# Optimization experiments

Measured on AMD Instinct MI355X. Metric: run time of the kernel, lower is better.

## Reference

```python
import jax, jax.numpy as jnp
import numpy as np

NUM_DISPARITIES = 64


def setup_inputs() -> dict:
    key = jax.random.key(0)
    k1, k2 = jax.random.split(key)
    B, C, H, W = 4, 32, 256, 512
    left = jax.random.normal(k1, (B, C, H, W), dtype=jnp.float32)
    right = jax.random.normal(k2, (B, C, H, W), dtype=jnp.float32)
    return {"left": left, "right": right}


def cost_volume(left, right, num_disparities):
    # left, right: [B, C, H, W] -> output [B, D, H, W]
    W = left.shape[3]
    wcoord = jnp.arange(W)  # [W]

    def one_disparity(i):
        # right shifted so rs[..., w] == right[..., w - i] for w >= i
        rs = jnp.roll(right, i, axis=3)
        corr = jnp.mean(left * rs, axis=1)  # [B, H, W] channel-mean dot product
        # zero out invalid columns w < i (matches zeros-init + slice write in torch)
        return jnp.where(wcoord >= i, corr, jnp.zeros_like(corr))

    # sequential map over disparities keeps peak memory at one [B,C,H,W] product
    out = jax.lax.map(one_disparity, jnp.arange(num_disparities))  # [D, B, H, W]
    return jnp.transpose(out, (1, 0, 2, 3))  # [B, D, H, W]


def reference(left, right):
    return cost_volume(left, right, NUM_DISPARITIES)
```

## Files before the change

kernel.cpp:

```cpp
#include <hip/hip_runtime.h>


constexpr int Bn = 4, Cn = 32, Hn = 256, Wn = 512, Dn = 64;
constexpr int WT = 4, DT = 16;
constexpr int PAD = 64;
constexpr int STRIDE = PAD + Wn;
constexpr int HW = Hn * Wn;

__global__ __launch_bounds__(512, 4)
void cost_volume_kernel(const float* __restrict__ left,
                        const float* __restrict__ right,
                        float* __restrict__ out)
{
    __shared__ __align__(16) float Rs[Cn * STRIDE];

    const int tid = threadIdx.x;
    const int bh  = blockIdx.x;
    const int b   = bh >> 8;
    const int h   = bh & (Hn - 1);

    const float* Lrow = left  + (b * Cn * Hn + h) * Wn;
    const float* Rrow = right + (b * Cn * Hn + h) * Wn;

    {
        const int c  = tid >> 4;
        const int wq = (tid & 15) << 2;
        *reinterpret_cast<float4*>(&Rs[c * STRIDE + wq]) =
            make_float4(0.f, 0.f, 0.f, 0.f);
    }

    #pragma unroll
    for (int k = 0; k < 8; ++k) {
        const int f = tid + (k << 9);
        const int c = f >> 7;
        const int w = (f & 127) << 2;
        const float4 v = *reinterpret_cast<const float4*>(&Rrow[c * HW + w]);
        *reinterpret_cast<float4*>(&Rs[c * STRIDE + PAD + w]) = v;
    }
    __syncthreads();

    const int tw = tid & 127;
    const int td = tid >> 7;
    const int w0 = tw << 2;
    const int d0 = td << 4;
    const int rbase = PAD + w0 - d0 - 16;

    float acc[DT][WT];
    #pragma unroll
    for (int j = 0; j < DT; ++j)
        #pragma unroll
        for (int i = 0; i < WT; ++i)
            acc[j][i] = 0.f;

    for (int c = 0; c < Cn; ++c) {
        const float4 Lv = *reinterpret_cast<const float4*>(&Lrow[c * HW + w0]);
        const float lv[4] = {Lv.x, Lv.y, Lv.z, Lv.w};

        const float* rp = &Rs[c * STRIDE + rbase];
        float r[20];
        #pragma unroll
        for (int q = 0; q < 5; ++q)
            *reinterpret_cast<float4*>(&r[q * 4]) =
                *reinterpret_cast<const float4*>(&rp[q * 4]);

        #pragma unroll
        for (int j = 0; j < DT; ++j)
            #pragma unroll
            for (int i = 0; i < WT; ++i)
                acc[j][i] = fmaf(lv[i], r[16 + i - j], acc[j][i]);
    }

    constexpr float inv = 1.0f / 32.0f;
    float* op = out + ((b * Dn + d0) * Hn + h) * Wn + w0;
    #pragma unroll
    for (int j = 0; j < DT; ++j) {
        const float4 v = make_float4(acc[j][0] * inv, acc[j][1] * inv,
                                     acc[j][2] * inv, acc[j][3] * inv);
        *reinterpret_cast<float4*>(&op[j * HW]) = v;
    }
}

extern "C" void kernel_launch(void* const* d_in, const int* in_sizes, int n_in,
                              void* d_out, int out_size, void* d_ws, size_t ws_size,
                              hipStream_t stream) {
    const float* left  = (const float*)d_in[0];
    const float* right = (const float*)d_in[1];
    float* out = (float*)d_out;
    cost_volume_kernel<<<dim3(Bn * Hn), dim3(512), 0, stream>>>(left, right, out);
}
```

Before: 249.8 us.

## Pipeline per-wave right-row staging via direct global-to-LDS ring buffers

Replaces the block-wide load of the whole right row into shared memory, and the barrier that follows, with a private three-slot ring buffer for each wave. The ring is filled asynchronously with global_load_lds and synchronised with manual waitcnt instructions, so channel loads overlap the FMA loop and the left-row loads are prefetched two channels ahead. Each wave now covers a 256-wide half-row for 16 disparities. This cuts LDS use from about 74KB to about 37KB, which may allow more blocks per CU. In exchange, each wave redundantly loads the overlapping halo, and correctness depends on the hand-written vmcnt and lgkmcnt counts.

```diff
diff --git a/kernel.cpp b/kernel.cpp
--- a/kernel.cpp
+++ b/kernel.cpp
@@ -2,82 +2,137 @@
 
 
 constexpr int Bn = 4, Cn = 32, Hn = 256, Wn = 512, Dn = 64;
-constexpr int WT = 4, DT = 16;
-constexpr int PAD = 64;
-constexpr int STRIDE = PAD + Wn;
 constexpr int HW = Hn * Wn;
+constexpr int SLOTF = 384;
+constexpr int NSLOT = 3;
+constexpr int WAVE_LDS = NSLOT * SLOTF;
+
+template<int NR>
+__device__ __forceinline__ void run_wave(
+    const float* __restrict__ Lrow, const float* __restrict__ Rrow,
+    float* __restrict__ out, float* ring,
+    const int lane, const int d0, const int wh, const int b, const int h)
+{
+    const int l4 = lane << 2;
+    const int w0 = wh + l4;
+
+    if (NR == 1) {
+        #pragma unroll
+        for (int k = 0; k < 2; ++k) {
+            const int idx = lane + (k << 6);
+            if (idx < NSLOT * 32) {
+                const int slot = idx >> 5;
+                const int o = (idx & 31) << 2;
+                *reinterpret_cast<float4*>(&ring[slot * SLOTF + o]) =
+                    make_float4(0.f, 0.f, 0.f, 0.f);
+            }
+        }
+    }
+
+    auto stageR = [&](int slot, int c) {
+        float* base = &ring[slot * SLOTF];
+        if constexpr (NR == 1) {
+            __builtin_amdgcn_global_load_lds(
+                (const __attribute__((address_space(1))) void*)(Rrow + c * HW + l4),
+                (__attribute__((address_space(3))) void*)(base + 128 + l4),
+                16, 0, 0);
+        } else {
+            __builtin_amdgcn_global_load_lds(
+                (const __attribute__((address_space(1))) void*)(Rrow + c * HW + 128 + l4),
+                (__attribute__((address_space(3))) void*)(base + l4),
+                16, 0, 0);
+            __builtin_amdgcn_global_load_lds(
+                (const __attribute__((address_space(1))) void*)(Rrow + c * HW + 256 + l4),
+                (__attribute__((address_space(3))) void*)(base + 128 + l4),
+                16, 0, 0);
+        }
+    };
+
+    float4 Lpf[NSLOT];
+    auto loadL = [&](int slot, int c) {
+        Lpf[slot] = *reinterpret_cast<const float4*>(&Lrow[c * HW + w0]);
+    };
+
+    float acc[16][4];
+    #pragma unroll
+    for (int j = 0; j < 16; ++j)
+        #pragma unroll
+        for (int i = 0; i < 4; ++i)
+            acc[j][i] = 0.f;
+
+    const int rbase = l4 + 112 - d0;
+
+    auto compute = [&](int slot) {
+        const float* Sb = &ring[slot * SLOTF];
+        float r[20];
+        #pragma unroll
+        for (int q = 0; q < 5; ++q)
+            *reinterpret_cast<float4*>(&r[q * 4]) =
+                *reinterpret_cast<const float4*>(&Sb[rbase + q * 4]);
+        const float4 Lv = Lpf[slot];
+        #pragma unroll
+        for (int j = 0; j < 16; ++j) {
+            acc[j][0] = fmaf(Lv.x, r[16 - j], acc[j][0]);
+            acc[j][1] = fmaf(Lv.y, r[17 - j], acc[j][1]);
+            acc[j][2] = fmaf(Lv.z, r[18 - j], acc[j][2]);
+            acc[j][3] = fmaf(Lv.w, r[19 - j], acc[j][3]);
+        }
+    };
+
+    stageR(0, 0); loadL(0, 0);
+    stageR(1, 1); loadL(1, 1);
+
+    #pragma unroll
+    for (int c = 0; c < Cn - 2; ++c) {
+        asm volatile("s_waitcnt lgkmcnt(0)" ::: "memory");
+        stageR((c + 2) % NSLOT, c + 2);
+        loadL((c + 2) % NSLOT, c + 2);
+        if constexpr (NR == 1) asm volatile("s_waitcnt vmcnt(4)" ::: "memory");
+        else                   asm volatile("s_waitcnt vmcnt(6)" ::: "memory");
+        compute(c % NSLOT);
+    }
+    if constexpr (NR == 1) asm volatile("s_waitcnt vmcnt(2)" ::: "memory");
+    else                   asm volatile("s_waitcnt vmcnt(3)" ::: "memory");
+    compute((Cn - 2) % NSLOT);
+    asm volatile("s_waitcnt vmcnt(0)" ::: "memory");
+    compute((Cn - 1) % NSLOT);
+
+    constexpr float inv = 1.0f / 32.0f;
+    float* op = out + ((b * Dn + d0) * Hn + h) * Wn + w0;
+    #pragma unroll
+    for (int j = 0; j < 16; ++j)
+        *reinterpret_cast<float4*>(&op[j * HW]) =
+            make_float4(acc[j][0] * inv, acc[j][1] * inv,
+                        acc[j][2] * inv, acc[j][3] * inv);
+}
 
 __global__ __launch_bounds__(512, 4)
 void cost_volume_kernel(const float* __restrict__ left,
                         const float* __restrict__ right,
                         float* __restrict__ out)
 {
-    __shared__ __align__(16) float Rs[Cn * STRIDE];
+    __shared__ __align__(16) float Rs[8 * WAVE_LDS];
 
-    const int tid = threadIdx.x;
-    const int bh  = blockIdx.x;
-    const int b   = bh >> 8;
-    const int h   = bh & (Hn - 1);
+    const int tid  = threadIdx.x;
+    const int wv   = tid >> 6;
+    const int lane = tid & 63;
+    const int dq   = wv & 3;
+    const int whi  = wv >> 2;
+    const int d0   = dq << 4;
+    const int wh   = whi << 8;
+
+    const int bh = blockIdx.x;
+    const int b  = bh >> 8;
+    const int h  = bh & (Hn - 1);
 
     const float* Lrow = left  + (b * Cn * Hn + h) * Wn;
     const float* Rrow = right + (b * Cn * Hn + h) * Wn;
+    float* ring = &Rs[wv * WAVE_LDS];
 
-    {
-        const int c  = tid >> 4;
-        const int wq = (tid & 15) << 2;
-        *reinterpret_cast<float4*>(&Rs[c * STRIDE + wq]) =
-            make_float4(0.f, 0.f, 0.f, 0.f);
-    }
-
-    #pragma unroll
-    for (int k = 0; k < 8; ++k) {
-        const int f = tid + (k << 9);
-        const int c = f >> 7;
-        const int w = (f & 127) << 2;
-        const float4 v = *reinterpret_cast<const float4*>(&Rrow[c * HW + w]);
-        *reinterpret_cast<float4*>(&Rs[c * STRIDE + PAD + w]) = v;
-    }
-    __syncthreads();
-
-    const int tw = tid & 127;
-    const int td = tid >> 7;
-    const int w0 = tw << 2;
-    const int d0 = td << 4;
-    const int rbase = PAD + w0 - d0 - 16;
-
-    float acc[DT][WT];
-    #pragma unroll
-    for (int j = 0; j < DT; ++j)
-        #pragma unroll
-        for (int i = 0; i < WT; ++i)
-            acc[j][i] = 0.f;
-
-    for (int c = 0; c < Cn; ++c) {
-        const float4 Lv = *reinterpret_cast<const float4*>(&Lrow[c * HW + w0]);
-        const float lv[4] = {Lv.x, Lv.y, Lv.z, Lv.w};
-
-        const float* rp = &Rs[c * STRIDE + rbase];
-        float r[20];
-        #pragma unroll
-        for (int q = 0; q < 5; ++q)
-            *reinterpret_cast<float4*>(&r[q * 4]) =
-                *reinterpret_cast<const float4*>(&rp[q * 4]);
-
-        #pragma unroll
-        for (int j = 0; j < DT; ++j)
-            #pragma unroll
-            for (int i = 0; i < WT; ++i)
-                acc[j][i] = fmaf(lv[i], r[16 + i - j], acc[j][i]);
-    }
-
-    constexpr float inv = 1.0f / 32.0f;
-    float* op = out + ((b * Dn + d0) * Hn + h) * Wn + w0;
-    #pragma unroll
-    for (int j = 0; j < DT; ++j) {
-        const float4 v = make_float4(acc[j][0] * inv, acc[j][1] * inv,
-                                     acc[j][2] * inv, acc[j][3] * inv);
-        *reinterpret_cast<float4*>(&op[j * HW]) = v;
-    }
+    if (whi == 0)
+        run_wave<1>(Lrow, Rrow, out, ring, lane, d0, wh, b, h);
+    else
+        run_wave<2>(Lrow, Rrow, out, ring, lane, d0, wh, b, h);
 }
 
 extern "C" void kernel_launch(void* const* d_in, const int* in_sizes, int n_in,
```

Result: slower. 308.3 us (+23.4%).
